# Kernel tuning notes

Measured on AMD Instinct MI355X. Metric: run time of the kernel, lower is better.

The kernel has to match this reference:

```python
import jax, jax.numpy as jnp
import numpy as np

B, C, L = 4, 512, 4096

def setup_inputs() -> dict:
    key = jax.random.key(0)
    k1, k2, k3, k4 = jax.random.split(key, 4)
    proj_query = jax.random.normal(k1, (B, C, L), dtype=jnp.float32)
    proj_key = jax.random.normal(k2, (B, C, L), dtype=jnp.float32)
    proj_val = jax.random.normal(k3, (B, C, L), dtype=jnp.float32)
    # binary padding mask over key positions, broadcast over query axis
    padding_mask = (jax.random.uniform(k4, (B, 1, L)) < 0.9).astype(jnp.float32)
    return {"proj_query": proj_query, "proj_key": proj_key,
            "proj_val": proj_val, "padding_mask": padding_mask}

def reference(proj_query, proj_key, proj_val, padding_mask):
    c = proj_query.shape[1]
    # energy[b,i,j] = sum_c Q[b,c,i] * K[b,c,j]  -> (B, L1, L2)
    energy = jnp.einsum('bci,bcj->bij', proj_query, proj_key)
    attention = energy / jnp.sqrt(jnp.asarray(c, dtype=energy.dtype))
    attention = attention + jnp.log(padding_mask + 1e-6)
    attention = jax.nn.softmax(attention, axis=-1)
    attention = attention * padding_mask
    attention = attention.transpose(0, 2, 1)  # (B, L2, L1)
    out = jnp.einsum('bcj,bji->bci', proj_val, attention)  # (B, C, L1)
    return out, attention
```

## Files before the change

### kernel.cpp

```cpp
#include <hip/hip_runtime.h>

#define B_ 4
#define C_ 512
#define L_ 4096

typedef __attribute__((ext_vector_type(8))) short bf16x8;
typedef __attribute__((ext_vector_type(4))) float f32x4;

static __device__ __forceinline__ unsigned short f2bf_rne(float f) {
  unsigned u = __float_as_uint(f);
  u += 0x7FFFu + ((u >> 16) & 1u);
  return (unsigned short)(u >> 16);
}
static __device__ __forceinline__ unsigned pack_rne(float a, float b) {
  return (unsigned)f2bf_rne(a) | ((unsigned)f2bf_rne(b) << 16);
}
static __device__ __forceinline__ float bflo2f(unsigned w) {
  return __uint_as_float(w << 16);
}
static __device__ __forceinline__ float bfhi2f(unsigned w) {
  return __uint_as_float(w & 0xFFFF0000u);
}

static __device__ __forceinline__ void g2lds16(const unsigned short* g,
                                               unsigned short* l) {
  __builtin_amdgcn_global_load_lds(
      (const __attribute__((address_space(1))) unsigned int*)g,
      (__attribute__((address_space(3))) unsigned int*)l, 16, 0, 0);
}

__global__ __launch_bounds__(256) void transpose_cast_k(
    const float* __restrict__ Q, const float* __restrict__ K,
    unsigned short* __restrict__ Qt, unsigned short* __restrict__ Kt) {
  int zb = blockIdx.z;
  int b = zb >> 1;
  const float* src = ((zb & 1) ? K : Q) + (size_t)b * C_ * L_;
  unsigned short* dst = ((zb & 1) ? Kt : Qt) + (size_t)b * L_ * C_;
  int i0 = blockIdx.x * 64, c0 = blockIdx.y * 64;
  __shared__ float tile[64][65];
  int t = threadIdx.x;
  int cr = t >> 2, ig = (t & 3) * 16;
  const float* s = src + (size_t)(c0 + cr) * L_ + i0 + ig;
#pragma unroll
  for (int q = 0; q < 4; ++q) {
    float4 v = *(const float4*)(s + 4 * q);
    tile[cr][ig + 4 * q + 0] = v.x;
    tile[cr][ig + 4 * q + 1] = v.y;
    tile[cr][ig + 4 * q + 2] = v.z;
    tile[cr][ig + 4 * q + 3] = v.w;
  }
  __syncthreads();
  int ir = t >> 2, cg = (t & 3) * 16;
  unsigned wds[8];
#pragma unroll
  for (int k = 0; k < 8; ++k)
    wds[k] = pack_rne(tile[cg + 2 * k][ir], tile[cg + 2 * k + 1][ir]);
  unsigned short* d = dst + (size_t)(i0 + ir) * C_ + c0 + cg;
  uint4 o0, o1;
  o0.x = wds[0]; o0.y = wds[1]; o0.z = wds[2]; o0.w = wds[3];
  o1.x = wds[4]; o1.y = wds[5]; o1.z = wds[6]; o1.w = wds[7];
  *(uint4*)d = o0;
  *(uint4*)(d + 8) = o1;
}

__global__ __launch_bounds__(256) void cast_v_k(
    const float* __restrict__ V, const float* __restrict__ mask,
    unsigned short* __restrict__ Vb) {
  size_t idx = ((size_t)blockIdx.x * 256 + threadIdx.x) * 8;
  int b = (int)(idx >> 21);
  int j = (int)(idx & (L_ - 1));
  float4 v0 = *(const float4*)(V + idx);
  float4 v1 = *(const float4*)(V + idx + 4);
  const float* m = mask + (size_t)b * L_ + j;
  float4 m0 = *(const float4*)m;
  float4 m1 = *(const float4*)(m + 4);
  uint4 o;
  o.x = pack_rne(v0.x * m0.x, v0.y * m0.y);
  o.y = pack_rne(v0.z * m0.z, v0.w * m0.w);
  o.z = pack_rne(v1.x * m1.x, v1.y * m1.y);
  o.w = pack_rne(v1.z * m1.z, v1.w * m1.w);
  *(uint4*)(Vb + idx) = o;
}

__device__ __forceinline__ void gemm_mainloop64(
    const unsigned short* Ab, const unsigned short* Bb, int lda, int ldb,
    int Kdim, unsigned short* sA, unsigned short* sB, f32x4 acc[4][4]) {
  int t = threadIdx.x;
  const unsigned short* pA[4];
  const unsigned short* pB[4];
#pragma unroll
  for (int c = 0; c < 4; ++c) {
    int e = t * 8 + c * 2048;
    int kc = e >> 12;
    int rem = e & 4095;
    int row = rem >> 5;
    int col = rem & 31;
    int off = kc * 32 + col;
    pA[c] = Ab + (size_t)row * lda + off;
    pB[c] = Bb + (size_t)row * ldb + off;
  }
  int lane = t & 63;
  int quad = lane >> 4;
  int l15 = lane & 15;
  int w = t >> 6;
  int wm = (w & 1) * 64;
  int wn = (w >> 1) * 64;
  for (int kk = 0; kk < Kdim; kk += 64) {
    __syncthreads();
#pragma unroll
    for (int c = 0; c < 4; ++c) g2lds16(pA[c] + kk, sA + t * 8 + c * 2048);
#pragma unroll
    for (int c = 0; c < 4; ++c) g2lds16(pB[c] + kk, sB + t * 8 + c * 2048);
    __syncthreads();
#pragma unroll
    for (int kc = 0; kc < 2; ++kc) {
      bf16x8 aF[4], bF[4];
#pragma unroll
      for (int ti = 0; ti < 4; ++ti)
        aF[ti] = *(const bf16x8*)(sA + kc * 4096 +
                                  (wm + ti * 16 + l15) * 32 + quad * 8);
#pragma unroll
      for (int tj = 0; tj < 4; ++tj)
        bF[tj] = *(const bf16x8*)(sB + kc * 4096 +
                                  (wn + tj * 16 + l15) * 32 + quad * 8);
#pragma unroll
      for (int ti = 0; ti < 4; ++ti)
#pragma unroll
        for (int tj = 0; tj < 4; ++tj)
          acc[ti][tj] = __builtin_amdgcn_mfma_f32_16x16x32_bf16(
              aF[ti], bF[tj], acc[ti][tj], 0, 0, 0);
    }
  }
}

__global__ __launch_bounds__(256) void gemm1_bf_k(
    const unsigned short* __restrict__ Qt, const unsigned short* __restrict__ Kt,
    const float* __restrict__ mask, unsigned short* __restrict__ t0,
    unsigned short* __restrict__ t1, unsigned short* __restrict__ t2,
    unsigned short* __restrict__ t3, float* __restrict__ rowsum) {
  int b = blockIdx.z;
  unsigned short* tbb = (b == 0) ? t0 : (b == 1) ? t1 : (b == 2) ? t2 : t3;
  int i0 = blockIdx.y * 128;
  int j0 = blockIdx.x * 128;
  __shared__ unsigned short sA[8192];
  __shared__ unsigned short sB[8192];
  f32x4 acc[4][4] = {};
  gemm_mainloop64(Qt + (size_t)b * L_ * C_ + (size_t)i0 * C_,
                  Kt + (size_t)b * L_ * C_ + (size_t)j0 * C_, C_, C_, C_, sA,
                  sB, acc);
  int t = threadIdx.x;
  int lane = t & 63;
  int quad = lane >> 4;
  int l15 = lane & 15;
  int w = t >> 6;
  int wm = (w & 1) * 64;
  int wn = (w >> 1) * 64;
  const float scale = 0.04419417382415922f;
  float lm[4], mv[4];
#pragma unroll
  for (int tj = 0; tj < 4; ++tj) {
    int j = j0 + wn + tj * 16 + l15;
    float m = mask[(size_t)b * L_ + j];
    mv[tj] = m;
    lm[tj] = __logf(m + 1e-6f);
  }
  float rs[16];
#pragma unroll
  for (int q = 0; q < 16; ++q) rs[q] = 0.f;
#pragma unroll
  for (int ti = 0; ti < 4; ++ti) {
    int irow = i0 + wm + ti * 16 + quad * 4;
#pragma unroll
    for (int r = 0; r < 4; ++r) {
      size_t ro = (size_t)(irow + r) * L_;
#pragma unroll
      for (int tj = 0; tj < 4; ++tj) {
        float x = fminf(acc[ti][tj][r] * scale + lm[tj], 60.f);
        float tv = __expf(x);
        rs[ti * 4 + r] += tv;
        tbb[ro + j0 + wn + tj * 16 + l15] = f2bf_rne(tv * mv[tj]);
      }
    }
  }
#pragma unroll
  for (int m = 1; m < 16; m <<= 1)
#pragma unroll
    for (int q = 0; q < 16; ++q) rs[q] += __shfl_xor(rs[q], m, 64);
  if (l15 == 0) {
    float* rb = rowsum + (size_t)b * L_ + i0 + wm;
#pragma unroll
    for (int ti = 0; ti < 4; ++ti)
#pragma unroll
      for (int r = 0; r < 4; ++r)
        atomicAdd(&rb[ti * 16 + quad * 4 + r], rs[ti * 4 + r]);
  }
}

template <bool ATOMIC>
__global__ __launch_bounds__(256) void gemm2_bf_k(
    const unsigned short* __restrict__ Vb, const unsigned short* __restrict__ t0,
    const unsigned short* __restrict__ t1, const unsigned short* __restrict__ t2,
    const unsigned short* __restrict__ t3, const float* __restrict__ rowsum,
    float* __restrict__ out, float* __restrict__ out2) {
  int z = blockIdx.z;
  int b = z & 3;
  int ks = z >> 2;
  const unsigned short* tbb =
      (b == 0) ? t0 : (b == 1) ? t1 : (b == 2) ? t2 : t3;
  int c0 = blockIdx.y * 128;
  int i0 = blockIdx.x * 128;
  __shared__ unsigned short sA[8192];
  __shared__ unsigned short sB[8192];
  f32x4 acc[4][4] = {};
  gemm_mainloop64(Vb + (size_t)b * C_ * L_ + (size_t)c0 * L_ + ks * (L_ / 2),
                  tbb + (size_t)i0 * L_ + ks * (L_ / 2), L_, L_, L_ / 2, sA, sB,
                  acc);
  int t = threadIdx.x;
  int lane = t & 63;
  int quad = lane >> 4;
  int l15 = lane & 15;
  int w = t >> 6;
  int wm = (w & 1) * 64;
  int wn = (w >> 1) * 64;
  float invv[4];
#pragma unroll
  for (int tj = 0; tj < 4; ++tj)
    invv[tj] = 1.0f / rowsum[(size_t)b * L_ + i0 + wn + tj * 16 + l15];
  float* ob = (ATOMIC ? out : (ks ? out2 : out)) + (size_t)b * C_ * L_;
#pragma unroll
  for (int ti = 0; ti < 4; ++ti) {
    int crow = c0 + wm + ti * 16 + quad * 4;
#pragma unroll
    for (int r = 0; r < 4; ++r) {
      size_t ro = (size_t)(crow + r) * L_;
#pragma unroll
      for (int tj = 0; tj < 4; ++tj) {
        float v = acc[ti][tj][r] * invv[tj];
        if (ATOMIC)
          atomicAdd(&ob[ro + i0 + wn + tj * 16 + l15], v);
        else
          ob[ro + i0 + wn + tj * 16 + l15] = v;
      }
    }
  }
}

__global__ __launch_bounds__(256) void combine_out_k(
    float* __restrict__ out, const float* __restrict__ out2) {
  size_t idx = ((size_t)blockIdx.x * 256 + threadIdx.x) * 8;
  float4 a0 = *(const float4*)(out + idx);
  float4 a1 = *(const float4*)(out + idx + 4);
  float4 b0 = *(const float4*)(out2 + idx);
  float4 b1 = *(const float4*)(out2 + idx + 4);
  a0.x += b0.x; a0.y += b0.y; a0.z += b0.z; a0.w += b0.w;
  a1.x += b1.x; a1.y += b1.y; a1.z += b1.z; a1.w += b1.w;
  *(float4*)(out + idx) = a0;
  *(float4*)(out + idx + 4) = a1;
}

__global__ __launch_bounds__(256) void finalize_all_k(
    const unsigned short* __restrict__ tb, const float* __restrict__ rowsum,
    float* __restrict__ attn) {
  int b = blockIdx.z;
  const unsigned short* src = tb + (size_t)b * L_ * L_;
  const float* rs = rowsum + (size_t)b * L_;
  float* dst = attn + (size_t)b * L_ * L_;
  int jt = blockIdx.x, it = blockIdx.y;
  __shared__ float tileT[64][65];
  int t = threadIdx.x;
  int r = t >> 2, cg = (t & 3) * 16;
  int i = it * 64 + r;
  float inv = 1.0f / rs[i];
  const unsigned short* sp = src + (size_t)i * L_ + jt * 64 + cg;
  uint4 u0 = *(const uint4*)sp;
  uint4 u1 = *(const uint4*)(sp + 8);
  const unsigned* w0 = (const unsigned*)&u0;
  const unsigned* w1 = (const unsigned*)&u1;
#pragma unroll
  for (int k = 0; k < 4; ++k) {
    tileT[cg + 2 * k + 0][r] = bflo2f(w0[k]) * inv;
    tileT[cg + 2 * k + 1][r] = bfhi2f(w0[k]) * inv;
    tileT[cg + 8 + 2 * k + 0][r] = bflo2f(w1[k]) * inv;
    tileT[cg + 8 + 2 * k + 1][r] = bfhi2f(w1[k]) * inv;
  }
  __syncthreads();
  float* dp = dst + (size_t)(jt * 64 + r) * L_ + it * 64 + cg;
#pragma unroll
  for (int q = 0; q < 4; ++q) {
    float4 o;
    o.x = tileT[r][cg + 4 * q + 0];
    o.y = tileT[r][cg + 4 * q + 1];
    o.z = tileT[r][cg + 4 * q + 2];
    o.w = tileT[r][cg + 4 * q + 3];
    *(float4*)(dp + 4 * q) = o;
  }
}

extern "C" void kernel_launch(void* const* d_in, const int* in_sizes, int n_in,
                              void* d_out, int out_size, void* d_ws,
                              size_t ws_size, hipStream_t stream) {
  const float* Q = (const float*)d_in[0];
  const float* K = (const float*)d_in[1];
  const float* V = (const float*)d_in[2];
  const float* mask = (const float*)d_in[3];

  float* out = (float*)d_out;
  float* attn = out + (size_t)B_ * C_ * L_;

  const size_t NQ = (size_t)B_ * L_ * C_;
  const size_t SLOT = (size_t)L_ * L_;
  unsigned short* Qt = (unsigned short*)d_ws;
  unsigned short* Kt = Qt + NQ;
  unsigned short* Vb = Kt + NQ;
  float* rowsum = (float*)(Vb + NQ);
  unsigned short* wtail = (unsigned short*)(rowsum + (size_t)B_ * L_);

  const size_t need1 =
      NQ * 2 * 3 + (size_t)B_ * L_ * 4 + (size_t)B_ * SLOT * 2 + NQ * 4;

  hipMemsetAsync(rowsum, 0, (size_t)B_ * L_ * sizeof(float), stream);
  transpose_cast_k<<<dim3(L_ / 64, C_ / 64, B_ * 2), 256, 0, stream>>>(Q, K, Qt,
                                                                       Kt);
  cast_v_k<<<dim3((B_ * C_ * L_) / 2048), 256, 0, stream>>>(V, mask, Vb);

  if (ws_size >= need1) {
    unsigned short* tb = wtail;
    float* out2 = (float*)(tb + (size_t)B_ * SLOT);
    gemm1_bf_k<<<dim3(L_ / 128, L_ / 128, B_), 256, 0, stream>>>(
        Qt, Kt, mask, tb, tb + SLOT, tb + 2 * SLOT, tb + 3 * SLOT, rowsum);
    gemm2_bf_k<false><<<dim3(L_ / 128, C_ / 128, B_ * 2), 256, 0, stream>>>(
        Vb, tb, tb + SLOT, tb + 2 * SLOT, tb + 3 * SLOT, rowsum, out, out2);
    combine_out_k<<<dim3((B_ * C_ * L_) / 2048), 256, 0, stream>>>(out, out2);
    finalize_all_k<<<dim3(64, 64, B_), 256, 0, stream>>>(tb, rowsum, attn);
  } else {
    unsigned short* tb0 = (unsigned short*)(attn + 2 * SLOT);
    unsigned short* tb1 = (unsigned short*)(attn + 3 * SLOT);
    unsigned short* tb2 = (unsigned short*)(attn + 3 * SLOT + SLOT / 2);
    unsigned short* tb3 = wtail;
    hipMemsetAsync(out, 0, (size_t)B_ * C_ * L_ * sizeof(float), stream);
    gemm1_bf_k<<<dim3(L_ / 128, L_ / 128, B_), 256, 0, stream>>>(
        Qt, Kt, mask, tb0, tb1, tb2, tb3, rowsum);
    gemm2_bf_k<true><<<dim3(L_ / 128, C_ / 128, B_ * 2), 256, 0, stream>>>(
        Vb, tb0, tb1, tb2, tb3, rowsum, out, out);
    finalize_all_k<<<dim3(64, 64, 1), 256, 0, stream>>>(tb0, rowsum, attn);
    finalize_all_k<<<dim3(64, 64, 1), 256, 0, stream>>>(tb1, rowsum + L_,
                                                        attn + SLOT);
    finalize_all_k<<<dim3(64, 64, 1), 256, 0, stream>>>(tb2, rowsum + 2 * L_,
                                                        attn + 2 * SLOT);
    finalize_all_k<<<dim3(64, 64, 1), 256, 0, stream>>>(tb3, rowsum + 3 * L_,
                                                        attn + 3 * SLOT);
  }
}
```

Baseline: 668.7 us.

## Replace both GEMMs with 256x256-tile 8-phase pipelined MFMA kernels

Adds a new GEMM mainloop that uses 256x256 block tiles, 512 threads and double-buffered, XOR-swizzled LDS. Global-to-LDS staging is interleaved with MFMA phases through explicit barriers, waitcnts and s_setprio. Block indices are remapped for better L2 locality. Both the QK^T/softmax GEMM and the attention·V GEMM use the new kernels on the large-workspace path. The aims are higher MFMA utilisation and overlap of loads with compute, at the cost of many barriers and 128KB of LDS per block. That LDS use limits occupancy, and the hand-tuned waitcnt counts are fragile.

Measured after the change: 662.7 us. No clear change (-0.9%).

```diff
diff --git a/kernel.cpp b/kernel.cpp
--- a/kernel.cpp
+++ b/kernel.cpp
@@ -6,6 +6,8 @@
 
 typedef __attribute__((ext_vector_type(8))) short bf16x8;
 typedef __attribute__((ext_vector_type(4))) float f32x4;
+
+#define MFMA16(a, b, c) __builtin_amdgcn_mfma_f32_16x16x32_bf16(a, b, c, 0, 0, 0)
 
 static __device__ __forceinline__ unsigned short f2bf_rne(float f) {
   unsigned u = __float_as_uint(f);
@@ -82,6 +84,287 @@
   *(uint4*)(Vb + idx) = o;
 }
 
+__device__ __forceinline__ void gemm_8phase(
+    const unsigned short* __restrict__ Ab,
+    const unsigned short* __restrict__ Bb, int lda, int ldb, int Kdim,
+    unsigned short* sA, unsigned short* sB, f32x4 (&acc)[8][4]) {
+  const int t = threadIdx.x;
+  const int lane = t & 63;
+  const int quad = lane >> 4;
+  const int l15 = lane & 15;
+  const int w = t >> 6;
+  const int wm = (w & 1) * 128;
+  const int wn = (w >> 1) * 64;
+  const int et = (t * 8) ^ (((t >> 5) & 1) << 4);
+  const int srw = et >> 5;
+  const int scl = et & 31;
+  const int nt = Kdim >> 6;
+
+  auto stage = [&](int nom, int hh) {
+    int st = nom < nt ? nom : nt - 1;
+    int db = nom & 1;
+    int h = hh & 1;
+    const unsigned short* g;
+    unsigned short* l;
+    if (hh < 2) {
+      g = Bb + (size_t)(h * 128 + srw) * ldb + st * 64 + scl;
+      l = sB + db * 16384 + h * 4096 + t * 8;
+    } else {
+      g = Ab + (size_t)(h * 128 + srw) * lda + st * 64 + scl;
+      l = sA + db * 16384 + h * 4096 + t * 8;
+    }
+    g2lds16(g, l);
+    g2lds16(g + 32, l + 8192);
+  };
+  auto rd = [&](const unsigned short* s, int db, int kc, int row) -> bf16x8 {
+    int e = db * 16384 + kc * 8192 + row * 32 + quad * 8;
+    e ^= ((e >> 8) & 1) << 4;
+    return *(const bf16x8*)(s + e);
+  };
+
+  bf16x8 aF[4][2], b0[2][2], b1[2][2];
+  auto rdA4 = [&](int db, int mbase) {
+#pragma unroll
+    for (int m = 0; m < 4; ++m)
+#pragma unroll
+      for (int kc = 0; kc < 2; ++kc)
+        aF[m][kc] = rd(sA, db, kc, wm + (mbase + m) * 16 + l15);
+  };
+  auto rdB2 = [&](bf16x8 (&bf)[2][2], int db, int nbase) {
+#pragma unroll
+    for (int n = 0; n < 2; ++n)
+#pragma unroll
+      for (int kc = 0; kc < 2; ++kc)
+        bf[n][kc] = rd(sB, db, kc, wn + (nbase + n) * 16 + l15);
+  };
+  auto mfma8 = [&](bf16x8 (&bf)[2][2], int mo, int no) {
+    __builtin_amdgcn_s_setprio(1);
+#pragma unroll
+    for (int m = 0; m < 4; ++m)
+#pragma unroll
+      for (int n = 0; n < 2; ++n) {
+        acc[mo + m][no + n] = MFMA16(aF[m][0], bf[n][0], acc[mo + m][no + n]);
+        acc[mo + m][no + n] = MFMA16(aF[m][1], bf[n][1], acc[mo + m][no + n]);
+      }
+    __builtin_amdgcn_s_setprio(0);
+  };
+
+#define BAR_() __builtin_amdgcn_s_barrier()
+#define LGKM0_() asm volatile("s_waitcnt lgkmcnt(0)" ::: "memory")
+#define VM6_() asm volatile("s_waitcnt vmcnt(6)" ::: "memory")
+#define SCHED0_() __builtin_amdgcn_sched_barrier(0)
+
+  stage(0, 0); stage(0, 1); stage(0, 2); stage(0, 3);
+  asm volatile("s_waitcnt vmcnt(4)" ::: "memory");
+  stage(1, 0); stage(1, 1); stage(1, 2);
+  asm volatile("s_waitcnt vmcnt(6)" ::: "memory");
+  BAR_();
+
+  const int ni = nt >> 1;
+  for (int i = 0; i < ni; ++i) {
+    const int X = 2 * i;
+    rdA4(0, 0); rdB2(b0, 0, 0); rdB2(b1, 0, 2);
+    stage(X + 1, 3);
+    BAR_(); LGKM0_();
+    mfma8(b0, 0, 0);
+    BAR_();
+    stage(X + 2, 0);
+    BAR_();
+    mfma8(b1, 0, 2);
+    BAR_();
+    rdA4(0, 4);
+    stage(X + 2, 1);
+    BAR_(); LGKM0_();
+    mfma8(b0, 4, 0);
+    BAR_();
+    stage(X + 2, 2);
+    VM6_(); BAR_();
+    mfma8(b1, 4, 2);
+    BAR_(); SCHED0_();
+    rdA4(1, 0); rdB2(b0, 1, 0); rdB2(b1, 1, 2);
+    stage(X + 2, 3);
+    BAR_(); LGKM0_();
+    mfma8(b0, 0, 0);
+    BAR_();
+    stage(X + 3, 0);
+    BAR_();
+    mfma8(b1, 0, 2);
+    BAR_();
+    rdA4(1, 4);
+    stage(X + 3, 1);
+    BAR_(); LGKM0_();
+    mfma8(b0, 4, 0);
+    BAR_();
+    stage(X + 3, 2);
+    VM6_(); BAR_();
+    mfma8(b1, 4, 2);
+    BAR_(); SCHED0_();
+  }
+  asm volatile("s_waitcnt vmcnt(0)" ::: "memory");
+}
+
+__global__ __launch_bounds__(512, 2) void gemm1_8p_k(
+    const unsigned short* __restrict__ Qt, const unsigned short* __restrict__ Kt,
+    const float* __restrict__ mask, unsigned short* __restrict__ t0,
+    unsigned short* __restrict__ t1, unsigned short* __restrict__ t2,
+    unsigned short* __restrict__ t3, float* __restrict__ rowsum) {
+  __shared__ unsigned short sA[32768];
+  __shared__ unsigned short sB[32768];
+  int flat = blockIdx.x + (blockIdx.y << 4) + (blockIdx.z << 8);
+  int swz = (flat & 7) * 128 + (flat >> 3);
+  int bx = swz & 15, by = (swz >> 4) & 15, b = swz >> 8;
+  unsigned short* tbb = (b == 0) ? t0 : (b == 1) ? t1 : (b == 2) ? t2 : t3;
+  int i0 = by * 256, j0 = bx * 256;
+  f32x4 acc[8][4] = {};
+  gemm_8phase(Qt + (size_t)b * L_ * C_ + (size_t)i0 * C_,
+              Kt + (size_t)b * L_ * C_ + (size_t)j0 * C_, C_, C_, C_, sA, sB,
+              acc);
+  int t = threadIdx.x;
+  int lane = t & 63;
+  int quad = lane >> 4;
+  int l15 = lane & 15;
+  int w = t >> 6;
+  int wm = (w & 1) * 128;
+  int wn = (w >> 1) * 64;
+  const float scale = 0.04419417382415922f;
+  float lm[4], mv[4];
+#pragma unroll
+  for (int n = 0; n < 4; ++n) {
+    int j = j0 + wn + n * 16 + l15;
+    float m = mask[(size_t)b * L_ + j];
+    mv[n] = m;
+    lm[n] = __logf(m + 1e-6f);
+  }
+  float rs[8][4];
+#pragma unroll
+  for (int m = 0; m < 8; ++m)
+#pragma unroll
+    for (int r = 0; r < 4; ++r) rs[m][r] = 0.f;
+#pragma unroll
+  for (int m = 0; m < 8; ++m) {
+    int irow = i0 + wm + m * 16 + quad * 4;
+#pragma unroll
+    for (int r = 0; r < 4; ++r) {
+      size_t ro = (size_t)(irow + r) * L_;
+#pragma unroll
+      for (int n = 0; n < 4; ++n) {
+        float x = fminf(acc[m][n][r] * scale + lm[n], 60.f);
+        float tv = __expf(x);
+        rs[m][r] += tv;
+        tbb[ro + j0 + wn + n * 16 + l15] = f2bf_rne(tv * mv[n]);
+      }
+    }
+  }
+#pragma unroll
+  for (int mm = 1; mm < 16; mm <<= 1)
+#pragma unroll
+    for (int m = 0; m < 8; ++m)
+#pragma unroll
+      for (int r = 0; r < 4; ++r) rs[m][r] += __shfl_xor(rs[m][r], mm, 64);
+  if (l15 == 0) {
+    float* rb = rowsum + (size_t)b * L_ + i0 + wm;
+#pragma unroll
+    for (int m = 0; m < 8; ++m)
+#pragma unroll
+      for (int r = 0; r < 4; ++r)
+        atomicAdd(&rb[m * 16 + quad * 4 + r], rs[m][r]);
+  }
+}
+
+__global__ __launch_bounds__(512, 2) void gemm2_8p_k(
+    const unsigned short* __restrict__ Vb, const unsigned short* __restrict__ t0,
+    const unsigned short* __restrict__ t1, const unsigned short* __restrict__ t2,
+    const unsigned short* __restrict__ t3, const float* __restrict__ rowsum,
+    float* __restrict__ out, float* __restrict__ out2) {
+  __shared__ unsigned short sA[32768];
+  __shared__ unsigned short sB[32768];
+  int flat = blockIdx.x + (blockIdx.y << 4) + (blockIdx.z << 5);
+  int swz = (flat & 7) * 32 + (flat >> 3);
+  int ix = swz & 15, cy = (swz >> 4) & 1, z = swz >> 5;
+  int b = z & 3, ks = z >> 2;
+  const unsigned short* tbb =
+      (b == 0) ? t0 : (b == 1) ? t1 : (b == 2) ? t2 : t3;
+  int i0 = ix * 256, c0 = cy * 256;
+  f32x4 acc[8][4] = {};
+  gemm_8phase(Vb + (size_t)b * C_ * L_ + (size_t)c0 * L_ + ks * (L_ / 2),
+              tbb + (size_t)i0 * L_ + ks * (L_ / 2), L_, L_, L_ / 2, sA, sB,
+              acc);
+  int t = threadIdx.x;
+  int lane = t & 63;
+  int quad = lane >> 4;
+  int l15 = lane & 15;
+  int w = t >> 6;
+  int wm = (w & 1) * 128;
+  int wn = (w >> 1) * 64;
+  float invv[4];
+#pragma unroll
+  for (int n = 0; n < 4; ++n)
+    invv[n] = 1.0f / rowsum[(size_t)b * L_ + i0 + wn + n * 16 + l15];
+  float* ob = (ks ? out2 : out) + (size_t)b * C_ * L_;
+#pragma unroll
+  for (int m = 0; m < 8; ++m) {
+    int crow = c0 + wm + m * 16 + quad * 4;
+#pragma unroll
+    for (int r = 0; r < 4; ++r) {
+      size_t ro = (size_t)(crow + r) * L_;
+#pragma unroll
+      for (int n = 0; n < 4; ++n)
+        ob[ro + i0 + wn + n * 16 + l15] = acc[m][n][r] * invv[n];
+    }
+  }
+}
+
+__global__ __launch_bounds__(256) void combine_out_k(
+    float* __restrict__ out, const float* __restrict__ out2) {
+  size_t idx = ((size_t)blockIdx.x * 256 + threadIdx.x) * 8;
+  float4 a0 = *(const float4*)(out + idx);
+  float4 a1 = *(const float4*)(out + idx + 4);
+  float4 b0 = *(const float4*)(out2 + idx);
+  float4 b1 = *(const float4*)(out2 + idx + 4);
+  a0.x += b0.x; a0.y += b0.y; a0.z += b0.z; a0.w += b0.w;
+  a1.x += b1.x; a1.y += b1.y; a1.z += b1.z; a1.w += b1.w;
+  *(float4*)(out + idx) = a0;
+  *(float4*)(out + idx + 4) = a1;
+}
+
+__global__ __launch_bounds__(256) void finalize_all_k(
+    const unsigned short* __restrict__ tb, const float* __restrict__ rowsum,
+    float* __restrict__ attn) {
+  int b = blockIdx.z;
+  const unsigned short* src = tb + (size_t)b * L_ * L_;
+  const float* rs = rowsum + (size_t)b * L_;
+  float* dst = attn + (size_t)b * L_ * L_;
+  int jt = blockIdx.x, it = blockIdx.y;
+  __shared__ float tileT[64][65];
+  int t = threadIdx.x;
+  int r = t >> 2, cg = (t & 3) * 16;
+  int i = it * 64 + r;
+  float inv = 1.0f / rs[i];
+  const unsigned short* sp = src + (size_t)i * L_ + jt * 64 + cg;
+  uint4 u0 = *(const uint4*)sp;
+  uint4 u1 = *(const uint4*)(sp + 8);
+  const unsigned* w0 = (const unsigned*)&u0;
+  const unsigned* w1 = (const unsigned*)&u1;
+#pragma unroll
+  for (int k = 0; k < 4; ++k) {
+    tileT[cg + 2 * k + 0][r] = bflo2f(w0[k]) * inv;
+    tileT[cg + 2 * k + 1][r] = bfhi2f(w0[k]) * inv;
+    tileT[cg + 8 + 2 * k + 0][r] = bflo2f(w1[k]) * inv;
+    tileT[cg + 8 + 2 * k + 1][r] = bfhi2f(w1[k]) * inv;
+  }
+  __syncthreads();
+  float* dp = dst + (size_t)(jt * 64 + r) * L_ + it * 64 + cg;
+#pragma unroll
+  for (int q = 0; q < 4; ++q) {
+    float4 o;
+    o.x = tileT[r][cg + 4 * q + 0];
+    o.y = tileT[r][cg + 4 * q + 1];
+    o.z = tileT[r][cg + 4 * q + 2];
+    o.w = tileT[r][cg + 4 * q + 3];
+    *(float4*)(dp + 4 * q) = o;
+  }
+}
+
 __device__ __forceinline__ void gemm_mainloop64(
     const unsigned short* Ab, const unsigned short* Bb, int lda, int ldb,
     int Kdim, unsigned short* sA, unsigned short* sB, f32x4 acc[4][4]) {
@@ -127,8 +410,7 @@
       for (int ti = 0; ti < 4; ++ti)
 #pragma unroll
         for (int tj = 0; tj < 4; ++tj)
-          acc[ti][tj] = __builtin_amdgcn_mfma_f32_16x16x32_bf16(
-              aF[ti], bF[tj], acc[ti][tj], 0, 0, 0);
+          acc[ti][tj] = MFMA16(aF[ti], bF[tj], acc[ti][tj]);
     }
   }
 }
@@ -196,12 +478,11 @@
   }
 }
 
-template <bool ATOMIC>
 __global__ __launch_bounds__(256) void gemm2_bf_k(
     const unsigned short* __restrict__ Vb, const unsigned short* __restrict__ t0,
     const unsigned short* __restrict__ t1, const unsigned short* __restrict__ t2,
     const unsigned short* __restrict__ t3, const float* __restrict__ rowsum,
-    float* __restrict__ out, float* __restrict__ out2) {
+    float* __restrict__ out) {
   int z = blockIdx.z;
   int b = z & 3;
   int ks = z >> 2;
@@ -226,7 +507,7 @@
 #pragma unroll
   for (int tj = 0; tj < 4; ++tj)
     invv[tj] = 1.0f / rowsum[(size_t)b * L_ + i0 + wn + tj * 16 + l15];
-  float* ob = (ATOMIC ? out : (ks ? out2 : out)) + (size_t)b * C_ * L_;
+  float* ob = out + (size_t)b * C_ * L_;
 #pragma unroll
   for (int ti = 0; ti < 4; ++ti) {
     int crow = c0 + wm + ti * 16 + quad * 4;
@@ -234,65 +515,10 @@
     for (int r = 0; r < 4; ++r) {
       size_t ro = (size_t)(crow + r) * L_;
 #pragma unroll
-      for (int tj = 0; tj < 4; ++tj) {
-        float v = acc[ti][tj][r] * invv[tj];
-        if (ATOMIC)
-          atomicAdd(&ob[ro + i0 + wn + tj * 16 + l15], v);
-        else
-          ob[ro + i0 + wn + tj * 16 + l15] = v;
-      }
+      for (int tj = 0; tj < 4; ++tj)
+        atomicAdd(&ob[ro + i0 + wn + tj * 16 + l15],
+                  acc[ti][tj][r] * invv[tj]);
     }
-  }
-}
-
-__global__ __launch_bounds__(256) void combine_out_k(
-    float* __restrict__ out, const float* __restrict__ out2) {
-  size_t idx = ((size_t)blockIdx.x * 256 + threadIdx.x) * 8;
-  float4 a0 = *(const float4*)(out + idx);
-  float4 a1 = *(const float4*)(out + idx + 4);
-  float4 b0 = *(const float4*)(out2 + idx);
-  float4 b1 = *(const float4*)(out2 + idx + 4);
-  a0.x += b0.x; a0.y += b0.y; a0.z += b0.z; a0.w += b0.w;
-  a1.x += b1.x; a1.y += b1.y; a1.z += b1.z; a1.w += b1.w;
-  *(float4*)(out + idx) = a0;
-  *(float4*)(out + idx + 4) = a1;
-}
-
-__global__ __launch_bounds__(256) void finalize_all_k(
-    const unsigned short* __restrict__ tb, const float* __restrict__ rowsum,
-    float* __restrict__ attn) {
-  int b = blockIdx.z;
-  const unsigned short* src = tb + (size_t)b * L_ * L_;
-  const float* rs = rowsum + (size_t)b * L_;
-  float* dst = attn + (size_t)b * L_ * L_;
-  int jt = blockIdx.x, it = blockIdx.y;
-  __shared__ float tileT[64][65];
-  int t = threadIdx.x;
-  int r = t >> 2, cg = (t & 3) * 16;
-  int i = it * 64 + r;
-  float inv = 1.0f / rs[i];
-  const unsigned short* sp = src + (size_t)i * L_ + jt * 64 + cg;
-  uint4 u0 = *(const uint4*)sp;
-  uint4 u1 = *(const uint4*)(sp + 8);
-  const unsigned* w0 = (const unsigned*)&u0;
-  const unsigned* w1 = (const unsigned*)&u1;
-#pragma unroll
-  for (int k = 0; k < 4; ++k) {
-    tileT[cg + 2 * k + 0][r] = bflo2f(w0[k]) * inv;
-    tileT[cg + 2 * k + 1][r] = bfhi2f(w0[k]) * inv;
-    tileT[cg + 8 + 2 * k + 0][r] = bflo2f(w1[k]) * inv;
-    tileT[cg + 8 + 2 * k + 1][r] = bfhi2f(w1[k]) * inv;
-  }
-  __syncthreads();
-  float* dp = dst + (size_t)(jt * 64 + r) * L_ + it * 64 + cg;
-#pragma unroll
-  for (int q = 0; q < 4; ++q) {
-    float4 o;
-    o.x = tileT[r][cg + 4 * q + 0];
-    o.y = tileT[r][cg + 4 * q + 1];
-    o.z = tileT[r][cg + 4 * q + 2];
-    o.w = tileT[r][cg + 4 * q + 3];
-    *(float4*)(dp + 4 * q) = o;
   }
 }
 
@@ -326,9 +552,9 @@
   if (ws_size >= need1) {
     unsigned short* tb = wtail;
     float* out2 = (float*)(tb + (size_t)B_ * SLOT);
-    gemm1_bf_k<<<dim3(L_ / 128, L_ / 128, B_), 256, 0, stream>>>(
+    gemm1_8p_k<<<dim3(16, 16, B_), 512, 0, stream>>>(
         Qt, Kt, mask, tb, tb + SLOT, tb + 2 * SLOT, tb + 3 * SLOT, rowsum);
-    gemm2_bf_k<false><<<dim3(L_ / 128, C_ / 128, B_ * 2), 256, 0, stream>>>(
+    gemm2_8p_k<<<dim3(16, 2, B_ * 2), 512, 0, stream>>>(
         Vb, tb, tb + SLOT, tb + 2 * SLOT, tb + 3 * SLOT, rowsum, out, out2);
     combine_out_k<<<dim3((B_ * C_ * L_) / 2048), 256, 0, stream>>>(out, out2);
     finalize_all_k<<<dim3(64, 64, B_), 256, 0, stream>>>(tb, rowsum, attn);
@@ -340,8 +566,8 @@
     hipMemsetAsync(out, 0, (size_t)B_ * C_ * L_ * sizeof(float), stream);
     gemm1_bf_k<<<dim3(L_ / 128, L_ / 128, B_), 256, 0, stream>>>(
         Qt, Kt, mask, tb0, tb1, tb2, tb3, rowsum);
-    gemm2_bf_k<true><<<dim3(L_ / 128, C_ / 128, B_ * 2), 256, 0, stream>>>(
-        Vb, tb0, tb1, tb2, tb3, rowsum, out, out);
+    gemm2_bf_k<<<dim3(L_ / 128, C_ / 128, B_ * 2), 256, 0, stream>>>(
+        Vb, tb0, tb1, tb2, tb3, rowsum, out);
     finalize_all_k<<<dim3(64, 64, 1), 256, 0, stream>>>(tb0, rowsum, attn);
     finalize_all_k<<<dim3(64, 64, 1), 256, 0, stream>>>(tb1, rowsum + L_,
                                                         attn + SLOT);
```
